# Optimization experiments

Hardware: AMD Instinct MI355X
Metric: run time of the kernel (lower is better)

Reference implementation:

```python
import jax, jax.numpy as jnp
import numpy as np

REF_CHANNEL = 0
DIAG_EPS = 1e-7   # diag_loading coefficient
TIK_EPS = 1e-8    # additive eps in diagonal loading / trace denominator
MASK_EPS = 1e-15  # PSD mask-normalization eps


def _psd(spec, mask):
    # spec: (b, c, f, t) complex; mask: (b, f, t) real
    # PSD module: normalize mask over time, weight outer products, sum over t.
    m = mask / (mask.sum(axis=-1, keepdims=True) + MASK_EPS)
    return jnp.einsum('bcft,beft,bft->bfce', spec, spec.conj(), m.astype(spec.dtype))


def setup_inputs() -> dict:
    key = jax.random.key(0)
    k1, k2, k3, k4 = jax.random.split(key, 4)
    B, C, F, T = 4, 6, 257, 2000
    return {
        'spec_real': jax.random.normal(k1, (B, C, F, T), dtype=jnp.float32),
        'spec_imag': jax.random.normal(k2, (B, C, F, T), dtype=jnp.float32),
        'mask_s': jax.random.uniform(k3, (B, F, T), dtype=jnp.float32),
        'mask_n': jax.random.uniform(k4, (B, F, T), dtype=jnp.float32),
    }


def reference(spec_real, spec_imag, mask_s, mask_n):
    spec = spec_real + 1j * spec_imag                     # (b, c, f, t) complex64
    C = spec.shape[1]

    psd_s = _psd(spec, mask_s)                            # (b, f, c, c)
    psd_n = _psd(spec, mask_n)                            # (b, f, c, c)

    # Diagonal loading (Tikhonov regularization) of the noise PSD.
    tr_n = jnp.einsum('bfcc->bf', psd_n).real
    epsilon = jax.lax.stop_gradient(tr_n * DIAG_EPS + TIK_EPS)   # torch uses no_grad here
    psd_n = psd_n + epsilon[..., None, None] * jnp.eye(C, dtype=spec.dtype)

    # ref_channel solution: w = (psd_n^-1 psd_s) / trace(psd_n^-1 psd_s) @ u
    numerator = jnp.linalg.solve(psd_n, psd_s)            # (b, f, c, c)
    tr = jnp.einsum('bfcc->bf', numerator)
    ws = numerator / (tr[..., None, None] + TIK_EPS)
    w = ws[..., :, REF_CHANNEL]                           # one-hot u selects column -> (b, f, c)

    # enhanced = w^H Y
    enh = jnp.einsum('bfc,bcft->bft', w.conj(), spec)     # (b, f, t) complex
    return jnp.stack([enh.real, enh.imag], axis=-1)       # (b, f, t, 2) float32
```

## Files before the change

kernel.cpp:

```cpp
#include <hip/hip_runtime.h>

#define NB 4
#define NC 6
#define NF 257
#define NT 2000
#define NG (NB * NF)
#define NPAIR 15
#define NACC 74
#define NCHUNK 2
#define TCH (NT / NCHUNK)
#define NP4 (TCH / 4)
#define BLK 256
#define CS  (NF * NT)
#define CS4 (CS / 4)

typedef float nfloat4 __attribute__((ext_vector_type(4)));

template<int CTRL>
__device__ __forceinline__ float dpp_add(float v) {
    int s = __builtin_amdgcn_update_dpp(0, __builtin_bit_cast(int, v), CTRL, 0xF, 0xF, true);
    return v + __builtin_bit_cast(float, s);
}

__global__ __launch_bounds__(BLK) void psd_kernel(
    const float* __restrict__ sr, const float* __restrict__ si,
    const float* __restrict__ ms, const float* __restrict__ mn,
    float* __restrict__ wsp)
{
    constexpr int PC[NPAIR] = {0,0,0,0,0,1,1,1,1,2,2,2,3,3,4};
    constexpr int PE[NPAIR] = {1,2,3,4,5,2,3,4,5,3,4,5,4,5,5};

    const int bx = blockIdx.x;
    const int g  = bx >> 1;
    const int b  = g / NF;
    const int f  = g - b * NF;
    const int tb = (bx & 1) * TCH;
    const int sbase = b * NC * CS + f * NT + tb;
    const int mbase = g * NT + tb;

    const nfloat4* s4r = (const nfloat4*)(sr + sbase);
    const nfloat4* s4i = (const nfloat4*)(si + sbase);
    const nfloat4* m4s = (const nfloat4*)(ms + mbase);
    const nfloat4* m4n = (const nfloat4*)(mn + mbase);

    float acc[NACC];
    #pragma unroll
    for (int i = 0; i < NACC; i++) acc[i] = 0.f;

    const bool act = threadIdx.x < NP4;
    const int  p   = act ? threadIdx.x : 0;
    {
        float wms[4], wmn[4], rr[NC][4], ii[NC][4];
        {
            const nfloat4 t0 = m4s[p];
            wms[0] = t0.x; wms[1] = t0.y; wms[2] = t0.z; wms[3] = t0.w;
            const nfloat4 t1 = m4n[p];
            wmn[0] = t1.x; wmn[1] = t1.y; wmn[2] = t1.z; wmn[3] = t1.w;
        }
        #pragma unroll
        for (int c = 0; c < NC; c++) {
            const nfloat4 tr = s4r[c * CS4 + p];
            rr[c][0] = tr.x; rr[c][1] = tr.y; rr[c][2] = tr.z; rr[c][3] = tr.w;
            const nfloat4 ti = s4i[c * CS4 + p];
            ii[c][0] = ti.x; ii[c][1] = ti.y; ii[c][2] = ti.z; ii[c][3] = ti.w;
        }
        if (!act) {
            #pragma unroll
            for (int k = 0; k < 4; k++) { wms[k] = 0.f; wmn[k] = 0.f; }
        }
        #pragma unroll
        for (int k = 0; k < 4; k++) { acc[72] += wms[k]; acc[73] += wmn[k]; }
        #pragma unroll
        for (int c = 0; c < NC; c++) {
            #pragma unroll
            for (int k = 0; k < 4; k++) {
                const float d = rr[c][k] * rr[c][k] + ii[c][k] * ii[c][k];
                acc[c]     += d * wms[k];
                acc[6 + c] += d * wmn[k];
            }
        }
        #pragma unroll
        for (int q = 0; q < NPAIR; q++) {
            const int c = PC[q], e = PE[q];
            #pragma unroll
            for (int k = 0; k < 4; k++) {
                const float cr = rr[c][k] * rr[e][k] + ii[c][k] * ii[e][k];
                const float ci = ii[c][k] * rr[e][k] - rr[c][k] * ii[e][k];
                acc[12 + 4 * q + 0] += cr * wms[k];
                acc[12 + 4 * q + 1] += ci * wms[k];
                acc[12 + 4 * q + 2] += cr * wmn[k];
                acc[12 + 4 * q + 3] += ci * wmn[k];
            }
        }
    }

    #pragma unroll
    for (int i = 0; i < NACC; i++) {
        float v = acc[i];
        v = dpp_add<0x118>(v);
        v = dpp_add<0x114>(v);
        v = dpp_add<0x112>(v);
        acc[i] = v;
    }

    __shared__ float red[32][NACC];
    const int lane16 = threadIdx.x & 15;
    const int ridx   = ((threadIdx.x >> 4) << 1) | (lane16 & 1);
    if (lane16 >= 14) {
        #pragma unroll
        for (int i = 0; i < NACC; i++) red[ridx][i] = acc[i];
    }
    __syncthreads();

    if (threadIdx.x < NACC) {
        float s = 0.f;
        #pragma unroll
        for (int r = 0; r < 32; r++) s += red[r][threadIdx.x];
        wsp[bx * NACC + threadIdx.x] = s;
    }
}

__global__ __launch_bounds__(64, 1) void solve_kernel(
    const float* __restrict__ wsp, float* __restrict__ wsw)
{
    const int gid = blockIdx.x * 64 + threadIdx.x;
    if (gid >= NG) return;

    constexpr int PC[NPAIR] = {0,0,0,0,0,1,1,1,1,2,2,2,3,3,4};
    constexpr int PE[NPAIR] = {1,2,3,4,5,2,3,4,5,3,4,5,4,5,5};
    constexpr int QIDX[NC][NC] = {
        {-1, 0, 1, 2, 3, 4},
        {-1,-1, 5, 6, 7, 8},
        {-1,-1,-1, 9,10,11},
        {-1,-1,-1,-1,12,13},
        {-1,-1,-1,-1,-1,14},
        {-1,-1,-1,-1,-1,-1}};

    const float* p0 = wsp + (NCHUNK * gid) * NACC;
    float fin[NACC];
    #pragma unroll
    for (int i = 0; i < NACC; i++)
        fin[i] = p0[i] + p0[NACC + i];

    const float invS = 1.f / (fin[72] + 1e-15f);
    const float invN = 1.f / (fin[73] + 1e-15f);

    float Ar[NC][NC], Ai[NC][NC];
    #pragma unroll
    for (int c = 0; c < NC; c++) { Ar[c][c] = fin[6 + c] * invN; Ai[c][c] = 0.f; }
    #pragma unroll
    for (int q = 0; q < NPAIR; q++) {
        const int c = PC[q], e = PE[q];
        const float nre = fin[12 + 4 * q + 2] * invN;
        const float nim = fin[12 + 4 * q + 3] * invN;
        Ar[c][e] = nre;  Ai[c][e] = nim;
        Ar[e][c] = nre;  Ai[e][c] = -nim;
    }
    {
        float trn = 0.f;
        #pragma unroll
        for (int c = 0; c < NC; c++) trn += Ar[c][c];
        const float eps = trn * 1e-7f + 1e-8f;
        #pragma unroll
        for (int c = 0; c < NC; c++) Ar[c][c] += eps;
    }

    #pragma unroll
    for (int k = 0; k < NC; k++) {
        const float dr = Ar[k][k], di = Ai[k][k];
        const float idn = 1.f / (dr * dr + di * di);
        const float pr = dr * idn, pi = -di * idn;
        #pragma unroll
        for (int i = k + 1; i < NC; i++) {
            const float lr = Ar[i][k] * pr - Ai[i][k] * pi;
            const float li = Ar[i][k] * pi + Ai[i][k] * pr;
            Ar[i][k] = lr; Ai[i][k] = li;
            #pragma unroll
            for (int j = k + 1; j < NC; j++) {
                Ar[i][j] -= lr * Ar[k][j] - li * Ai[k][j];
                Ai[i][j] -= lr * Ai[k][j] + li * Ar[k][j];
            }
        }
    }

    float trr = 1e-8f, tri = 0.f;
    float w0r[NC], w0i[NC];
    #pragma unroll
    for (int j = 0; j < NC; j++) {
        float xr[NC], xi[NC];
        #pragma unroll
        for (int i = 0; i < NC; i++) {
            if (i == j)      { xr[i] = fin[j] * invS;                      xi[i] = 0.f; }
            else if (i < j)  { const int q = QIDX[i][j];
                               xr[i] = fin[12 + 4 * q] * invS;  xi[i] =  fin[13 + 4 * q] * invS; }
            else             { const int q = QIDX[j][i];
                               xr[i] = fin[12 + 4 * q] * invS;  xi[i] = -fin[13 + 4 * q] * invS; }
        }
        #pragma unroll
        for (int i = 1; i < NC; i++) {
            #pragma unroll
            for (int k = 0; k < NC - 1; k++) if (k < i) {
                xr[i] -= Ar[i][k] * xr[k] - Ai[i][k] * xi[k];
                xi[i] -= Ar[i][k] * xi[k] + Ai[i][k] * xr[k];
            }
        }
        #pragma unroll
        for (int i = NC - 1; i >= 0; i--) {
            #pragma unroll
            for (int k = 0; k < NC; k++) if (k > i) {
                xr[i] -= Ar[i][k] * xr[k] - Ai[i][k] * xi[k];
                xi[i] -= Ar[i][k] * xi[k] + Ai[i][k] * xr[k];
            }
            const float dr = Ar[i][i], di = Ai[i][i];
            const float idn = 1.f / (dr * dr + di * di);
            const float pr = dr * idn, pi = -di * idn;
            const float tr0 = xr[i] * pr - xi[i] * pi;
            xi[i] = xr[i] * pi + xi[i] * pr;
            xr[i] = tr0;
        }
        trr += xr[j]; tri += xi[j];
        if (j == 0) {
            #pragma unroll
            for (int i = 0; i < NC; i++) { w0r[i] = xr[i]; w0i[i] = xi[i]; }
        }
    }

    const float idn = 1.f / (trr * trr + tri * tri);
    #pragma unroll
    for (int c = 0; c < NC; c++) {
        const float wre = (w0r[c] * trr + w0i[c] * tri) * idn;
        const float wim = (w0i[c] * trr - w0r[c] * tri) * idn;
        wsw[gid * 12 + c]     = wre;
        wsw[gid * 12 + 6 + c] = -wim;
    }
}

__global__ __launch_bounds__(BLK) void apply_kernel(
    const float* __restrict__ sr, const float* __restrict__ si,
    const float* __restrict__ wsw, float* __restrict__ out)
{
    const int bx = blockIdx.x;
    const int g  = bx >> 1;
    const int b  = g / NF;
    const int f  = g - b * NF;
    const int tb = (bx & 1) * TCH;
    const int sbase = b * NC * CS + f * NT + tb;

    const nfloat4* s4r = (const nfloat4*)(sr + sbase);
    const nfloat4* s4i = (const nfloat4*)(si + sbase);

    float wr[NC], wi[NC];
    #pragma unroll
    for (int c = 0; c < NC; c++) {
        wr[c] = wsw[g * 12 + c];
        wi[c] = wsw[g * 12 + 6 + c];
    }

    nfloat4* o4 = (nfloat4*)(out + 2 * (g * NT + tb));

    const int p = threadIdx.x;
    if (p < NP4) {
        float rr[NC][4], ii[NC][4];
        #pragma unroll
        for (int c = 0; c < NC; c++) {
            const nfloat4 tr = s4r[c * CS4 + p];
            rr[c][0] = tr.x; rr[c][1] = tr.y; rr[c][2] = tr.z; rr[c][3] = tr.w;
            const nfloat4 ti = s4i[c * CS4 + p];
            ii[c][0] = ti.x; ii[c][1] = ti.y; ii[c][2] = ti.z; ii[c][3] = ti.w;
        }
        float er[4], ei[4];
        #pragma unroll
        for (int k = 0; k < 4; k++) {
            float a = 0.f, bb = 0.f;
            #pragma unroll
            for (int c = 0; c < NC; c++) {
                a  += wr[c] * rr[c][k] - wi[c] * ii[c][k];
                bb += wr[c] * ii[c][k] + wi[c] * rr[c][k];
            }
            er[k] = a; ei[k] = bb;
        }
        nfloat4 o0 = {er[0], ei[0], er[1], ei[1]};
        nfloat4 o1 = {er[2], ei[2], er[3], ei[3]};
        __builtin_nontemporal_store(o0, &o4[2 * p]);
        __builtin_nontemporal_store(o1, &o4[2 * p + 1]);
    }
}

extern "C" void kernel_launch(void* const* d_in, const int* in_sizes, int n_in,
                              void* d_out, int out_size, void* d_ws, size_t ws_size,
                              hipStream_t stream) {
    const float* sr = (const float*)d_in[0];
    const float* si = (const float*)d_in[1];
    const float* ms = (const float*)d_in[2];
    const float* mn = (const float*)d_in[3];
    float* out = (float*)d_out;

    float* wsp = (float*)d_ws;
    float* wsw = wsp + NG * NCHUNK * NACC;

    psd_kernel<<<NG * NCHUNK, BLK, 0, stream>>>(sr, si, ms, mn, wsp);
    solve_kernel<<<(NG + 63) / 64, 64, 0, stream>>>(wsp, wsw);
    apply_kernel<<<NG * NCHUNK, BLK, 0, stream>>>(sr, si, wsw, out);
}
```

Before: 173.2 us.

## Split PSD kernel by mask and finer time chunks to shrink per-thread accumulators

The PSD kernel now launches four times as many blocks. Each block handles a quarter of the time axis and only one of the two masks, chosen by block parity. This cuts each thread's accumulators from 74 to 37 and its per-thread loads from float4 to float2, which should lower register pressure and raise occupancy and memory-level parallelism. The trade-off is that each spectrum element is now read by two blocks (once per mask), and the solve kernel has to sum eight partials per frequency instead of two. The apply kernel keeps its own two-chunk split through new constants.

```diff
diff --git a/kernel.cpp b/kernel.cpp
--- a/kernel.cpp
+++ b/kernel.cpp
@@ -7,12 +7,14 @@
 #define NG (NB * NF)
 #define NPAIR 15
 #define NACC 74
-#define NCHUNK 2
+#define NACCS 37
+#define PSTR 40
+#define NCHUNK 4
 #define TCH (NT / NCHUNK)
-#define NP4 (TCH / 4)
+#define NP2 (TCH / 2)
 #define BLK 256
 #define CS  (NF * NT)
-#define CS4 (CS / 4)
+#define CS2 (CS / 2)
 
 typedef float nfloat4 __attribute__((ext_vector_type(4)));
 
@@ -30,72 +32,66 @@
     constexpr int PC[NPAIR] = {0,0,0,0,0,1,1,1,1,2,2,2,3,3,4};
     constexpr int PE[NPAIR] = {1,2,3,4,5,2,3,4,5,3,4,5,4,5,5};
 
-    const int bx = blockIdx.x;
-    const int g  = bx >> 1;
+    const int bx     = blockIdx.x;
+    const int g      = bx >> 3;
+    const int rem    = bx & 7;
+    const int chunk  = rem >> 1;
+    const int parity = rem & 1;
     const int b  = g / NF;
     const int f  = g - b * NF;
-    const int tb = (bx & 1) * TCH;
+    const int tb = chunk * TCH;
     const int sbase = b * NC * CS + f * NT + tb;
     const int mbase = g * NT + tb;
 
-    const nfloat4* s4r = (const nfloat4*)(sr + sbase);
-    const nfloat4* s4i = (const nfloat4*)(si + sbase);
-    const nfloat4* m4s = (const nfloat4*)(ms + mbase);
-    const nfloat4* m4n = (const nfloat4*)(mn + mbase);
-
-    float acc[NACC];
-    #pragma unroll
-    for (int i = 0; i < NACC; i++) acc[i] = 0.f;
-
-    const bool act = threadIdx.x < NP4;
+    const float2* s2r = (const float2*)(sr + sbase);
+    const float2* s2i = (const float2*)(si + sbase);
+    const float2* m2  = (const float2*)((parity ? mn : ms) + mbase);
+
+    float acc[NACCS];
+    #pragma unroll
+    for (int i = 0; i < NACCS; i++) acc[i] = 0.f;
+
+    const bool act = threadIdx.x < NP2;
     const int  p   = act ? threadIdx.x : 0;
     {
-        float wms[4], wmn[4], rr[NC][4], ii[NC][4];
+        float wm[2], rr[NC][2], ii[NC][2];
         {
-            const nfloat4 t0 = m4s[p];
-            wms[0] = t0.x; wms[1] = t0.y; wms[2] = t0.z; wms[3] = t0.w;
-            const nfloat4 t1 = m4n[p];
-            wmn[0] = t1.x; wmn[1] = t1.y; wmn[2] = t1.z; wmn[3] = t1.w;
+            const float2 t0 = m2[p];
+            wm[0] = t0.x; wm[1] = t0.y;
         }
         #pragma unroll
         for (int c = 0; c < NC; c++) {
-            const nfloat4 tr = s4r[c * CS4 + p];
-            rr[c][0] = tr.x; rr[c][1] = tr.y; rr[c][2] = tr.z; rr[c][3] = tr.w;
-            const nfloat4 ti = s4i[c * CS4 + p];
-            ii[c][0] = ti.x; ii[c][1] = ti.y; ii[c][2] = ti.z; ii[c][3] = ti.w;
-        }
-        if (!act) {
-            #pragma unroll
-            for (int k = 0; k < 4; k++) { wms[k] = 0.f; wmn[k] = 0.f; }
-        }
-        #pragma unroll
-        for (int k = 0; k < 4; k++) { acc[72] += wms[k]; acc[73] += wmn[k]; }
+            const float2 tr = s2r[c * CS2 + p];
+            rr[c][0] = tr.x; rr[c][1] = tr.y;
+            const float2 ti = s2i[c * CS2 + p];
+            ii[c][0] = ti.x; ii[c][1] = ti.y;
+        }
+        if (!act) { wm[0] = wm[1] = 0.f; }
+        #pragma unroll
+        for (int k = 0; k < 2; k++) acc[36] += wm[k];
         #pragma unroll
         for (int c = 0; c < NC; c++) {
             #pragma unroll
-            for (int k = 0; k < 4; k++) {
+            for (int k = 0; k < 2; k++) {
                 const float d = rr[c][k] * rr[c][k] + ii[c][k] * ii[c][k];
-                acc[c]     += d * wms[k];
-                acc[6 + c] += d * wmn[k];
+                acc[c] += d * wm[k];
             }
         }
         #pragma unroll
         for (int q = 0; q < NPAIR; q++) {
             const int c = PC[q], e = PE[q];
             #pragma unroll
-            for (int k = 0; k < 4; k++) {
+            for (int k = 0; k < 2; k++) {
                 const float cr = rr[c][k] * rr[e][k] + ii[c][k] * ii[e][k];
                 const float ci = ii[c][k] * rr[e][k] - rr[c][k] * ii[e][k];
-                acc[12 + 4 * q + 0] += cr * wms[k];
-                acc[12 + 4 * q + 1] += ci * wms[k];
-                acc[12 + 4 * q + 2] += cr * wmn[k];
-                acc[12 + 4 * q + 3] += ci * wmn[k];
-            }
-        }
-    }
-
-    #pragma unroll
-    for (int i = 0; i < NACC; i++) {
+                acc[6 + 2 * q]     += cr * wm[k];
+                acc[6 + 2 * q + 1] += ci * wm[k];
+            }
+        }
+    }
+
+    #pragma unroll
+    for (int i = 0; i < NACCS; i++) {
         float v = acc[i];
         v = dpp_add<0x118>(v);
         v = dpp_add<0x114>(v);
@@ -103,20 +99,20 @@
         acc[i] = v;
     }
 
-    __shared__ float red[32][NACC];
+    __shared__ float red[32][NACCS];
     const int lane16 = threadIdx.x & 15;
     const int ridx   = ((threadIdx.x >> 4) << 1) | (lane16 & 1);
     if (lane16 >= 14) {
         #pragma unroll
-        for (int i = 0; i < NACC; i++) red[ridx][i] = acc[i];
+        for (int i = 0; i < NACCS; i++) red[ridx][i] = acc[i];
     }
     __syncthreads();
 
-    if (threadIdx.x < NACC) {
+    if (threadIdx.x < NACCS) {
         float s = 0.f;
         #pragma unroll
         for (int r = 0; r < 32; r++) s += red[r][threadIdx.x];
-        wsp[bx * NACC + threadIdx.x] = s;
+        wsp[bx * PSTR + threadIdx.x] = s;
     }
 }
 
@@ -136,11 +132,25 @@
         {-1,-1,-1,-1,-1,14},
         {-1,-1,-1,-1,-1,-1}};
 
-    const float* p0 = wsp + (NCHUNK * gid) * NACC;
+    const float* p0 = wsp + (8 * gid) * PSTR;
+    float fs[NACCS], fn[NACCS];
+    #pragma unroll
+    for (int i = 0; i < NACCS; i++) {
+        fs[i] = (p0[0 * PSTR + i] + p0[2 * PSTR + i]) + (p0[4 * PSTR + i] + p0[6 * PSTR + i]);
+        fn[i] = (p0[1 * PSTR + i] + p0[3 * PSTR + i]) + (p0[5 * PSTR + i] + p0[7 * PSTR + i]);
+    }
     float fin[NACC];
     #pragma unroll
-    for (int i = 0; i < NACC; i++)
-        fin[i] = p0[i] + p0[NACC + i];
+    for (int c = 0; c < NC; c++) { fin[c] = fs[c]; fin[6 + c] = fn[c]; }
+    #pragma unroll
+    for (int q = 0; q < NPAIR; q++) {
+        fin[12 + 4 * q + 0] = fs[6 + 2 * q];
+        fin[12 + 4 * q + 1] = fs[6 + 2 * q + 1];
+        fin[12 + 4 * q + 2] = fn[6 + 2 * q];
+        fin[12 + 4 * q + 3] = fn[6 + 2 * q + 1];
+    }
+    fin[72] = fs[36];
+    fin[73] = fn[36];
 
     const float invS = 1.f / (fin[72] + 1e-15f);
     const float invN = 1.f / (fin[73] + 1e-15f);
@@ -234,6 +244,11 @@
         wsw[gid * 12 + 6 + c] = -wim;
     }
 }
+
+#define ACHUNK 2
+#define ATCH (NT / ACHUNK)
+#define ANP4 (ATCH / 4)
+#define CS4 (CS / 4)
 
 __global__ __launch_bounds__(BLK) void apply_kernel(
     const float* __restrict__ sr, const float* __restrict__ si,
@@ -243,7 +258,7 @@
     const int g  = bx >> 1;
     const int b  = g / NF;
     const int f  = g - b * NF;
-    const int tb = (bx & 1) * TCH;
+    const int tb = (bx & 1) * ATCH;
     const int sbase = b * NC * CS + f * NT + tb;
 
     const nfloat4* s4r = (const nfloat4*)(sr + sbase);
@@ -259,7 +274,7 @@
     nfloat4* o4 = (nfloat4*)(out + 2 * (g * NT + tb));
 
     const int p = threadIdx.x;
-    if (p < NP4) {
+    if (p < ANP4) {
         float rr[NC][4], ii[NC][4];
         #pragma unroll
         for (int c = 0; c < NC; c++) {
@@ -296,9 +311,9 @@
     float* out = (float*)d_out;
 
     float* wsp = (float*)d_ws;
-    float* wsw = wsp + NG * NCHUNK * NACC;
-
-    psd_kernel<<<NG * NCHUNK, BLK, 0, stream>>>(sr, si, ms, mn, wsp);
+    float* wsw = wsp + NG * 8 * PSTR;
+
+    psd_kernel<<<NG * NCHUNK * 2, BLK, 0, stream>>>(sr, si, ms, mn, wsp);
     solve_kernel<<<(NG + 63) / 64, 64, 0, stream>>>(wsp, wsw);
-    apply_kernel<<<NG * NCHUNK, BLK, 0, stream>>>(sr, si, wsw, out);
-}
+    apply_kernel<<<NG * ACHUNK, BLK, 0, stream>>>(sr, si, wsw, out);
+}
```

Result: no change. 174.4 us (+0.7%).
